# Performance work log

Hardware: AMD Instinct MI355X
Metric: run time of the kernel (lower is better)

The kernel has to match this reference:

```python
import jax, jax.numpy as jnp
import numpy as np

B, L, D = 8, 256, 32      # batch, key seq_len, input_dim
E, H, Q = 128, 8, 128     # embed_time, heads, num_query_steps
HID = 256                 # hidden_dim
V = 2 * D                 # value dim with mask channel
EK = E // H


def setup_inputs() -> dict:
    key = jax.random.key(0)
    ks = jax.random.split(key, 12)
    s = 0.05
    return {
        "values": jax.random.normal(ks[0], (B, L, D), jnp.float32),
        "mask": jax.random.randint(ks[1], (B, L, D), 0, 2).astype(jnp.int32),
        "times": jax.random.uniform(ks[2], (B, L), jnp.float32),
        # learn_time_embedding params (torch Linear(1, E-1) and Linear(1, 1))
        "w_per": jax.random.normal(ks[3], (1, E - 1), jnp.float32) * s,
        "b_per": jax.random.normal(ks[4], (E - 1,), jnp.float32) * s,
        "w_lin": jax.random.normal(ks[5], (1, 1), jnp.float32) * s,
        "b_lin": jax.random.normal(ks[6], (1,), jnp.float32) * s,
        # mTAND q/k linears (E,E) and output proj (HID, H*V)
        "wq": jax.random.normal(ks[7], (E, E), jnp.float32) * s,
        "bq": jnp.zeros((E,), jnp.float32),
        "wk": jax.random.normal(ks[8], (E, E), jnp.float32) * s,
        "bk": jnp.zeros((E,), jnp.float32),
        "wo": jax.random.normal(ks[9], (HID, H * V), jnp.float32) * s,
        "bo": jnp.zeros((HID,), jnp.float32),
        "ln_g": jnp.ones((HID,), jnp.float32),
        "ln_b": jnp.zeros((HID,), jnp.float32),
    }


def reference(values, mask, times, w_per, b_per, w_lin, b_lin,
              wq, bq, wk, bk, wo, bo, ln_g, ln_b):
    eps = 1e-6
    maskf = mask.astype(jnp.float32)                      # [B,L,D]
    obs = maskf.max(axis=-1) > 0                          # [B,L] observed steps
    # --- normalize times over observed steps ---
    tmin = jnp.where(obs, times, jnp.inf).min(axis=1, keepdims=True)
    tmax = jnp.where(obs, times, -jnp.inf).max(axis=1, keepdims=True)
    has = jnp.any(obs, axis=1, keepdims=True)             # [B,1]
    tmin = jnp.where(has, tmin, 0.0)
    tmax = jnp.where(has, tmax, 1.0)
    tn = (times - tmin) / jnp.maximum(tmax - tmin, eps)
    tn = jnp.where(obs, tn, 0.0)
    qt = jnp.broadcast_to(jnp.linspace(0.0, 1.0, Q, dtype=jnp.float32), (B, Q))

    def temb(tt):  # learnable time embedding: [linear(t), sin(periodic(t))]
        t = tt[..., None]                                 # [...,1]
        return jnp.concatenate([t @ w_lin.T + b_lin,
                                jnp.sin(t @ w_per + b_per)], axis=-1)

    tk = temb(tn)   # [B,L,E]
    tq = temb(qt)   # [B,Q,E]

    vinp = jnp.concatenate([values, maskf], axis=-1)      # [B,L,V]
    am = jnp.concatenate([maskf, maskf], axis=-1)         # [B,L,V]

    q = (tq @ wq.T + bq).reshape(B, Q, H, EK).transpose(0, 2, 1, 3)  # [B,H,Q,ek]
    k = (tk @ wk.T + bk).reshape(B, L, H, EK).transpose(0, 2, 1, 3)  # [B,H,L,ek]
    scores = jnp.einsum('bhqe,bhke->bhqk', q, k) / np.float32(np.sqrt(EK))
    # per-value-channel masked scores: [B,H,Q,L,V]
    s5 = jnp.where(am[:, None, None, :, :] == 0, jnp.float32(-10000.0),
                   scores[..., None])
    attn = jax.nn.softmax(s5, axis=-2)                    # softmax over L
    ctx = jnp.einsum('bhqkv,bkv->bhqv', attn, vinp)       # [B,H,Q,V]
    ctx = ctx.transpose(0, 2, 1, 3).reshape(B, Q, H * V)
    seq = ctx @ wo.T + bo                                 # [B,Q,HID]
    # LayerNorm (torch default eps=1e-5, biased var)
    mu = seq.mean(axis=-1, keepdims=True)
    var = ((seq - mu) ** 2).mean(axis=-1, keepdims=True)
    seq = (seq - mu) / jnp.sqrt(var + 1e-5) * ln_g + ln_b
    seq = seq * has.astype(jnp.float32)[:, :, None]       # zero seqs with no obs
    pooled = seq.mean(axis=1)
    return seq, pooled, qt
```

## Files before the change

### kernel.cpp

```cpp
#include <hip/hip_runtime.h>
#include <hip/hip_bf16.h>

#define B_   8
#define L_   256
#define D_   32
#define E_   128
#define H_   8
#define Q_   128
#define HID_ 256

__device__ __forceinline__ unsigned pack_bf2(float a, float b)
{
    __hip_bfloat16 ha = __float2bfloat16(a);
    __hip_bfloat16 hb = __float2bfloat16(b);
    unsigned short ua = *reinterpret_cast<unsigned short*>(&ha);
    unsigned short ub = *reinterpret_cast<unsigned short*>(&hb);
    return (unsigned)ua | ((unsigned)ub << 16);
}

__global__ __launch_bounds__(256) void k_prep1(
    const float* __restrict__ values, const int* __restrict__ mask,
    const float* __restrict__ times,
    float* __restrict__ tn, float* __restrict__ has,
    float* __restrict__ cm, float* __restrict__ colmean,
    float* __restrict__ mvm, unsigned* __restrict__ bitsT,
    float* __restrict__ qt_out, float* __restrict__ pooled)
{
    __shared__ float val_s[256][33];
    __shared__ unsigned bits_s[256];
    __shared__ float partial_s[8][32];
    __shared__ float sminw[4], smaxw[4];
    __shared__ float sh[2];

    int b = blockIdx.x;
    int t = threadIdx.x;

    const int*   mrow = mask   + (size_t)(b * L_ + t) * D_;
    const float* vrow = values + (size_t)(b * L_ + t) * D_;
    int4  m4[8];
    float4 v4[8];
    int any = 0;
    #pragma unroll
    for (int j = 0; j < 8; ++j) {
        m4[j] = reinterpret_cast<const int4*>(mrow)[j];
        v4[j] = reinterpret_cast<const float4*>(vrow)[j];
        any |= m4[j].x | m4[j].y | m4[j].z | m4[j].w;
        float4 mv;
        mv.x = m4[j].x ? v4[j].x : 0.f;
        mv.y = m4[j].y ? v4[j].y : 0.f;
        mv.z = m4[j].z ? v4[j].z : 0.f;
        mv.w = m4[j].w ? v4[j].w : 0.f;
        reinterpret_cast<float4*>(mvm + (size_t)(b * L_ + t) * D_)[j] = mv;
        val_s[t][j * 4 + 0] = v4[j].x;
        val_s[t][j * 4 + 1] = v4[j].y;
        val_s[t][j * 4 + 2] = v4[j].z;
        val_s[t][j * 4 + 3] = v4[j].w;
    }
    int wave = t >> 6;
    #pragma unroll
    for (int d = 0; d < D_; ++d) {
        int comp;
        { int j = d >> 2, c = d & 3;
          int4 mm = m4[j];
          comp = (c == 0) ? mm.x : (c == 1) ? mm.y : (c == 2) ? mm.z : mm.w; }
        unsigned long long bal = __ballot(comp != 0);
        if ((t & 63) == 0) {
            bits_s[d * 8 + wave * 2 + 0] = (unsigned)(bal & 0xffffffffull);
            bits_s[d * 8 + wave * 2 + 1] = (unsigned)(bal >> 32);
        }
    }
    float tv = times[b * L_ + t];
    {
        float wmin = any ? tv : 1e38f;
        float wmax = any ? tv : -1e38f;
        #pragma unroll
        for (int off = 32; off > 0; off >>= 1) {
            wmin = fminf(wmin, __shfl_xor(wmin, off));
            wmax = fmaxf(wmax, __shfl_xor(wmax, off));
        }
        if ((t & 63) == 0) { sminw[wave] = wmin; smaxw[wave] = wmax; }
    }
    {
        int d = t & 31, lg = t >> 5;
        float ps = 0.f;
        #pragma unroll
        for (int i = 0; i < 32; ++i) ps += val_s[lg * 32 + i][d];
        partial_s[lg][d] = ps;
    }
    __syncthreads();
    if (t == 0) {
        float mn = fminf(fminf(sminw[0], sminw[1]), fminf(sminw[2], sminw[3]));
        float mx = fmaxf(fmaxf(smaxw[0], smaxw[1]), fmaxf(smaxw[2], smaxw[3]));
        float hv = (mn < 1e37f) ? 1.f : 0.f;
        sh[0] = (hv > 0.f) ? mn : 0.f;
        sh[1] = (hv > 0.f) ? mx : 1.f;
        has[b] = hv;
    }
    __syncthreads();
    float inv = 1.f / fmaxf(sh[1] - sh[0], 1e-6f);
    tn[b * L_ + t] = any ? (tv - sh[0]) * inv : 0.f;

    if (t < Q_) qt_out[b * Q_ + t] = (float)t * (1.f / 127.f);
    pooled[b * HID_ + t] = 0.f;
    bitsT[b * 256 + t] = bits_s[t];

    if (t < D_) {
        float s = 0.f;
        #pragma unroll
        for (int lg = 0; lg < 8; ++lg) s += partial_s[lg][t];
        colmean[b * D_ + t] = s * (1.f / (float)L_);
        unsigned o = 0;
        #pragma unroll
        for (int w = 0; w < 8; ++w) o |= bits_s[t * 8 + w];
        cm[b * D_ + t] = o ? 1.f : 0.f;
    }
}

__global__ __launch_bounds__(256) void k_prep2(
    const float* __restrict__ tn, const float* __restrict__ cm,
    const float* __restrict__ w_per, const float* __restrict__ b_per,
    const float* __restrict__ w_lin, const float* __restrict__ b_lin,
    const float* __restrict__ wq, const float* __restrict__ bq,
    const float* __restrict__ wk, const float* __restrict__ bk,
    const float* __restrict__ wo, const float* __restrict__ bo,
    float* __restrict__ qproj, float* __restrict__ kproj,
    unsigned* __restrict__ wotvh, float* __restrict__ cvec)
{
    __shared__ __align__(16) float emb_q[2][E_];
    __shared__ __align__(16) float emb_k[8][E_];
    __shared__ float tsh[8];
    __shared__ float cm_s[D_];

    int blk = blockIdx.x;
    int t = threadIdx.x;

    if (blk < 64) {
        int half = t >> 7, e = t & 127;
        int q = blk * 2 + half;
        float tt = (float)q * (1.f / 127.f);
        emb_q[half][e] = (e == 0) ? (tt * w_lin[0] + b_lin[0])
                                  : __sinf(tt * w_per[e - 1] + b_per[e - 1]);
        __syncthreads();
        const float4* wr4 = reinterpret_cast<const float4*>(wq + (size_t)e * E_);
        const float4* e4  = reinterpret_cast<const float4*>(emb_q[half]);
        float acc = bq[e];
        #pragma unroll 8
        for (int j = 0; j < E_ / 4; ++j) {
            float4 w = wr4[j], x = e4[j];
            acc += w.x * x.x + w.y * x.y + w.z * x.z + w.w * x.w;
        }
        qproj[q * E_ + e] = acc;
    } else if (blk < 320) {
        int bl0 = (blk - 64) * 8;
        int e = t & 127, rh = t >> 7;
        if (t < 8) tsh[t] = tn[bl0 + t];
        __syncthreads();
        float wp = (e == 0) ? 0.f : w_per[e - 1];
        float bp = (e == 0) ? 0.f : b_per[e - 1];
        float wl = w_lin[0], bl = b_lin[0];
        #pragma unroll
        for (int rr = 0; rr < 4; ++rr) {
            int r = rh * 4 + rr;
            float tt = tsh[r];
            emb_k[r][e] = (e == 0) ? (tt * wl + bl) : __sinf(tt * wp + bp);
        }
        __syncthreads();
        const float4* wr4 = reinterpret_cast<const float4*>(wk + (size_t)e * E_);
        float bias = bk[e];
        float acc[4] = {bias, bias, bias, bias};
        #pragma unroll 8
        for (int j = 0; j < E_ / 4; ++j) {
            float4 w = wr4[j];
            #pragma unroll
            for (int rr = 0; rr < 4; ++rr) {
                float4 x = *reinterpret_cast<const float4*>(&emb_k[rh * 4 + rr][j * 4]);
                acc[rr] += w.x * x.x + w.y * x.y + w.z * x.z + w.w * x.w;
            }
        }
        #pragma unroll
        for (int rr = 0; rr < 4; ++rr)
            kproj[(size_t)(bl0 + rh * 4 + rr) * E_ + e] = acc[rr];
    } else if (blk < 352) {
        int c20 = (blk - 320) * 4;
        #pragma unroll
        for (int j = 0; j < 4; ++j) {
            int c2 = c20 + j;
            int ca = 2 * c2, cb = 2 * c2 + 1;
            int cola = (ca >> 5) * 64 + (ca & 31);
            int colb = (cb >> 5) * 64 + (cb & 31);
            float a = wo[(size_t)t * 512 + cola];
            float b = wo[(size_t)t * 512 + colb];
            wotvh[(size_t)c2 * HID_ + t] = pack_bf2(a, b);
        }
    } else {
        int b = blk - 352;
        if (t < D_) cm_s[t] = cm[b * D_ + t];
        __syncthreads();
        int hid = t;
        const float4* wrow4 = reinterpret_cast<const float4*>(wo + (size_t)hid * 512);
        float accm = 0.f;
        #pragma unroll
        for (int h1 = 0; h1 < 8; ++h1) {
            #pragma unroll
            for (int j = 0; j < 8; ++j) {
                float4 w = wrow4[h1 * 16 + 8 + j];
                accm += cm_s[j * 4 + 0] * w.x + cm_s[j * 4 + 1] * w.y
                      + cm_s[j * 4 + 2] * w.z + cm_s[j * 4 + 3] * w.w;
            }
        }
        cvec[b * HID_ + hid] = bo[hid] + accm;
    }
}

__global__ __launch_bounds__(256, 4) void k_main(
    const float* __restrict__ qproj, const float* __restrict__ kproj,
    const float* __restrict__ mvm, const unsigned* __restrict__ bitsT,
    const float* __restrict__ cm, const float* __restrict__ colmean,
    const unsigned* __restrict__ wotvh, const float* __restrict__ cvec,
    const float* __restrict__ has,
    const float* __restrict__ ln_g, const float* __restrict__ ln_b,
    float* __restrict__ seq_out, float* __restrict__ pooled)
{
    int q = blockIdx.x, b = blockIdx.y;
    int tid = threadIdx.x;
    __shared__ __align__(16) float e_s[L_ * H_];
    __shared__ __align__(16) float qv_s[E_];
    __shared__ unsigned bits_s[256];
    __shared__ float gmax_s[H_];
    __shared__ __align__(8) float ctx_s[256];
    __shared__ float red_s[8];
    __shared__ float mu_rs[2];

    bits_s[tid] = bitsT[b * 256 + tid];
    if (tid < E_) qv_s[tid] = qproj[q * E_ + tid];
    __syncthreads();

    const float4* kr4 = reinterpret_cast<const float4*>(kproj + (size_t)(b * L_ + tid) * E_);
    const float4* qv4 = reinterpret_cast<const float4*>(qv_s);
    float s[H_];
    #pragma unroll
    for (int h = 0; h < H_; ++h) {
        float acc = 0.f;
        #pragma unroll
        for (int j = 0; j < 4; ++j) {
            float4 kk = kr4[h * 4 + j], qq = qv4[h * 4 + j];
            acc += kk.x * qq.x + kk.y * qq.y + kk.z * qq.z + kk.w * qq.w;
        }
        s[h] = acc * 0.25f;
    }
    {
        float4* er4 = reinterpret_cast<float4*>(&e_s[tid * 8]);
        er4[0] = *reinterpret_cast<float4*>(&s[0]);
        er4[1] = *reinterpret_cast<float4*>(&s[4]);
    }
    __syncthreads();
    {
        int h = tid >> 5, ln = tid & 31;
        float mx = -1e30f;
        #pragma unroll
        for (int j = 0; j < 8; ++j) mx = fmaxf(mx, e_s[(ln + j * 32) * 8 + h]);
        #pragma unroll
        for (int off = 16; off > 0; off >>= 1) mx = fmaxf(mx, __shfl_xor(mx, off));
        if (ln == 0) gmax_s[h] = mx;
    }
    __syncthreads();
    {
        float e8[H_];
        #pragma unroll
        for (int h = 0; h < H_; ++h) e8[h] = __expf(s[h] - gmax_s[h]);
        float4* er4 = reinterpret_cast<float4*>(&e_s[tid * 8]);
        er4[0] = *reinterpret_cast<float4*>(&e8[0]);
        er4[1] = *reinterpret_cast<float4*>(&e8[4]);
    }
    __syncthreads();

    {
        int lseg = tid >> 6, h = (tid >> 3) & 7, d4 = tid & 7;
        unsigned w0[4], w1[4];
        #pragma unroll
        for (int j = 0; j < 4; ++j) {
            int d = d4 * 4 + j;
            w0[j] = bits_s[d * 8 + lseg * 2 + 0];
            w1[j] = bits_s[d * 8 + lseg * 2 + 1];
        }
        float4 av  = {0.f, 0.f, 0.f, 0.f};
        float4 den = {0.f, 0.f, 0.f, 0.f};
        const float4* mvg = reinterpret_cast<const float4*>(mvm + (size_t)b * L_ * D_);
        int l0 = lseg * 64;
        #pragma unroll 8
        for (int i = 0; i < 32; ++i) {
            int l = l0 + i;
            float e = e_s[l * 8 + h];
            float4 m = mvg[l * 8 + d4];
            av.x += e * m.x; av.y += e * m.y; av.z += e * m.z; av.w += e * m.w;
            den.x += ((w0[0] >> i) & 1u) ? e : 0.f;
            den.y += ((w0[1] >> i) & 1u) ? e : 0.f;
            den.z += ((w0[2] >> i) & 1u) ? e : 0.f;
            den.w += ((w0[3] >> i) & 1u) ? e : 0.f;
        }
        #pragma unroll 8
        for (int i = 0; i < 32; ++i) {
            int l = l0 + 32 + i;
            float e = e_s[l * 8 + h];
            float4 m = mvg[l * 8 + d4];
            av.x += e * m.x; av.y += e * m.y; av.z += e * m.z; av.w += e * m.w;
            den.x += ((w1[0] >> i) & 1u) ? e : 0.f;
            den.y += ((w1[1] >> i) & 1u) ? e : 0.f;
            den.z += ((w1[2] >> i) & 1u) ? e : 0.f;
            den.w += ((w1[3] >> i) & 1u) ? e : 0.f;
        }
        __syncthreads();
        float4* p4 = reinterpret_cast<float4*>(e_s);
        p4[tid * 2 + 0] = av;
        p4[tid * 2 + 1] = den;
    }
    __syncthreads();
    {
        int hh = tid >> 5, dd = tid & 31, dg = dd >> 2, jj = dd & 3;
        float a = 0.f, dn = 0.f;
        #pragma unroll
        for (int ls = 0; ls < 4; ++ls) {
            int pt = ls * 64 + hh * 8 + dg;
            a  += e_s[pt * 8 + jj];
            dn += e_s[pt * 8 + 4 + jj];
        }
        float cmf = cm[b * D_ + dd];
        ctx_s[tid] = (cmf > 0.f) ? (a / dn) : colmean[b * D_ + dd];
    }
    __syncthreads();

    int hid = tid;
    float acc = cvec[b * HID_ + hid];
    #pragma unroll 8
    for (int c2 = 0; c2 < 128; ++c2) {
        unsigned u = wotvh[(size_t)c2 * HID_ + hid];
        float2 cc = *reinterpret_cast<const float2*>(&ctx_s[c2 * 2]);
        float w0 = __uint_as_float(u << 16);
        float w1 = __uint_as_float(u & 0xffff0000u);
        acc += cc.x * w0 + cc.y * w1;
    }

    int wave = hid >> 6;
    {
        float sum = acc, ssum = acc * acc;
        #pragma unroll
        for (int off = 32; off > 0; off >>= 1) {
            sum  += __shfl_xor(sum, off);
            ssum += __shfl_xor(ssum, off);
        }
        if ((hid & 63) == 0) { red_s[wave] = sum; red_s[4 + wave] = ssum; }
    }
    __syncthreads();
    if (hid == 0) {
        float S  = red_s[0] + red_s[1] + red_s[2] + red_s[3];
        float SS = red_s[4] + red_s[5] + red_s[6] + red_s[7];
        float mu = S * (1.f / HID_);
        float var = SS * (1.f / HID_) - mu * mu;
        mu_rs[0] = mu;
        mu_rs[1] = rsqrtf(var + 1e-5f);
    }
    __syncthreads();

    float outv = ((acc - mu_rs[0]) * mu_rs[1] * ln_g[hid] + ln_b[hid]) * has[b];
    seq_out[((size_t)(b * Q_ + q)) * HID_ + hid] = outv;
    atomicAdd(&pooled[b * HID_ + hid], outv * (1.f / (float)Q_));
}

extern "C" void kernel_launch(void* const* d_in, const int* in_sizes, int n_in,
                              void* d_out, int out_size, void* d_ws, size_t ws_size,
                              hipStream_t stream)
{
    const float* values = (const float*)d_in[0];
    const int*   mask   = (const int*)  d_in[1];
    const float* times  = (const float*)d_in[2];
    const float* w_per  = (const float*)d_in[3];
    const float* b_per  = (const float*)d_in[4];
    const float* w_lin  = (const float*)d_in[5];
    const float* b_lin  = (const float*)d_in[6];
    const float* wq     = (const float*)d_in[7];
    const float* bq     = (const float*)d_in[8];
    const float* wk     = (const float*)d_in[9];
    const float* bk     = (const float*)d_in[10];
    const float* wo     = (const float*)d_in[11];
    const float* bo     = (const float*)d_in[12];
    const float* ln_g   = (const float*)d_in[13];
    const float* ln_b   = (const float*)d_in[14];

    float* out     = (float*)d_out;
    float* seq_out = out;
    float* pooled  = out + 262144;
    float* qt_out  = out + 262144 + 2048;

    float* ws         = (float*)d_ws;
    float*    tn      = ws;
    float*    has     = ws + 2048;
    float*    cm      = ws + 2056;
    float*    colmean = ws + 2312;
    float*    qproj   = ws + 2568;
    unsigned* bitsT   = (unsigned*)(ws + 18952);
    float*    mvm     = ws + 21000;
    float*    kproj   = ws + 86536;
    float*    cvec    = ws + 348680;
    unsigned* wotvh   = (unsigned*)(ws + 350728);

    k_prep1<<<B_,           256, 0, stream>>>(values, mask, times,
                 tn, has, cm, colmean, mvm, bitsT, qt_out, pooled);
    k_prep2<<<360,          256, 0, stream>>>(tn, cm, w_per, b_per, w_lin, b_lin,
                 wq, bq, wk, bk, wo, bo, qproj, kproj, wotvh, cvec);
    k_main <<<dim3(Q_, B_), 256, 0, stream>>>(qproj, kproj, mvm, bitsT,
                 cm, colmean, wotvh, cvec, has, ln_g, ln_b, seq_out, pooled);
}
```

Measured before the change: 144.1 us.

## Process two query steps per block and stage value matrix in shared memory

The main kernel now runs 512 threads per block, each half handling one query step, so the grid is halved. The per-batch masked value matrix (32 KB) is copied into LDS once per block and read from there in the context accumulation instead of from global memory. Shared buffers for scores, context and LayerNorm reductions are duplicated per query. This raises LDS use to about 50 KB per block, which may reduce occupancy, and every block still loads the full value tile, the same amount of work as before.

```diff
diff --git a/kernel.cpp b/kernel.cpp
--- a/kernel.cpp
+++ b/kernel.cpp
@@ -212,7 +212,7 @@
     }
 }
 
-__global__ __launch_bounds__(256, 4) void k_main(
+__global__ __launch_bounds__(512, 4) void k_main(
     const float* __restrict__ qproj, const float* __restrict__ kproj,
     const float* __restrict__ mvm, const unsigned* __restrict__ bitsT,
     const float* __restrict__ cm, const float* __restrict__ colmean,
@@ -221,22 +221,30 @@
     const float* __restrict__ ln_g, const float* __restrict__ ln_b,
     float* __restrict__ seq_out, float* __restrict__ pooled)
 {
-    int q = blockIdx.x, b = blockIdx.y;
+    int qb = blockIdx.x, b = blockIdx.y;
     int tid = threadIdx.x;
-    __shared__ __align__(16) float e_s[L_ * H_];
-    __shared__ __align__(16) float qv_s[E_];
+    int qi = tid >> 8, t = tid & 255;
+    __shared__ __align__(16) float mvm_s[L_ * D_];
+    __shared__ __align__(16) float e_s[2][L_ * H_];
+    __shared__ __align__(16) float qv_s[2][E_];
     __shared__ unsigned bits_s[256];
-    __shared__ float gmax_s[H_];
-    __shared__ __align__(8) float ctx_s[256];
-    __shared__ float red_s[8];
-    __shared__ float mu_rs[2];
-
-    bits_s[tid] = bitsT[b * 256 + tid];
-    if (tid < E_) qv_s[tid] = qproj[q * E_ + tid];
-    __syncthreads();
-
-    const float4* kr4 = reinterpret_cast<const float4*>(kproj + (size_t)(b * L_ + tid) * E_);
-    const float4* qv4 = reinterpret_cast<const float4*>(qv_s);
+    __shared__ float gmax_s[16];
+    __shared__ __align__(16) float ctx_s[2][256];
+    __shared__ float red_s[2][8];
+    __shared__ float mu_rs[2][2];
+
+    {
+        const float4* src = reinterpret_cast<const float4*>(mvm + (size_t)b * L_ * D_);
+        float4* dst = reinterpret_cast<float4*>(mvm_s);
+        #pragma unroll
+        for (int j = 0; j < 4; ++j) dst[tid + j * 512] = src[tid + j * 512];
+        if (qi == 0) bits_s[t] = bitsT[b * 256 + t];
+        if (t < E_) qv_s[qi][t] = qproj[(qb * 2 + qi) * E_ + t];
+    }
+    __syncthreads();
+
+    const float4* kr4 = reinterpret_cast<const float4*>(kproj + (size_t)(b * L_ + t) * E_);
+    const float4* qv4 = reinterpret_cast<const float4*>(qv_s[qi]);
     float s[H_];
     #pragma unroll
     for (int h = 0; h < H_; ++h) {
@@ -249,33 +257,34 @@
         s[h] = acc * 0.25f;
     }
     {
-        float4* er4 = reinterpret_cast<float4*>(&e_s[tid * 8]);
+        float4* er4 = reinterpret_cast<float4*>(&e_s[qi][t * 8]);
         er4[0] = *reinterpret_cast<float4*>(&s[0]);
         er4[1] = *reinterpret_cast<float4*>(&s[4]);
     }
     __syncthreads();
     {
-        int h = tid >> 5, ln = tid & 31;
+        int g = tid >> 5, ln = tid & 31;
+        int gq = g >> 3, h = g & 7;
         float mx = -1e30f;
         #pragma unroll
-        for (int j = 0; j < 8; ++j) mx = fmaxf(mx, e_s[(ln + j * 32) * 8 + h]);
+        for (int j = 0; j < 8; ++j) mx = fmaxf(mx, e_s[gq][(ln + j * 32) * 8 + h]);
         #pragma unroll
         for (int off = 16; off > 0; off >>= 1) mx = fmaxf(mx, __shfl_xor(mx, off));
-        if (ln == 0) gmax_s[h] = mx;
+        if (ln == 0) gmax_s[g] = mx;
     }
     __syncthreads();
     {
         float e8[H_];
         #pragma unroll
-        for (int h = 0; h < H_; ++h) e8[h] = __expf(s[h] - gmax_s[h]);
-        float4* er4 = reinterpret_cast<float4*>(&e_s[tid * 8]);
+        for (int h = 0; h < H_; ++h) e8[h] = __expf(s[h] - gmax_s[qi * 8 + h]);
+        float4* er4 = reinterpret_cast<float4*>(&e_s[qi][t * 8]);
         er4[0] = *reinterpret_cast<float4*>(&e8[0]);
         er4[1] = *reinterpret_cast<float4*>(&e8[4]);
     }
     __syncthreads();
 
     {
-        int lseg = tid >> 6, h = (tid >> 3) & 7, d4 = tid & 7;
+        int lseg = t >> 6, h = (t >> 3) & 7, d4 = t & 7;
         unsigned w0[4], w1[4];
         #pragma unroll
         for (int j = 0; j < 4; ++j) {
@@ -285,13 +294,14 @@
         }
         float4 av  = {0.f, 0.f, 0.f, 0.f};
         float4 den = {0.f, 0.f, 0.f, 0.f};
-        const float4* mvg = reinterpret_cast<const float4*>(mvm + (size_t)b * L_ * D_);
+        const float4* mv4 = reinterpret_cast<const float4*>(mvm_s);
+        const float* ep = e_s[qi];
         int l0 = lseg * 64;
         #pragma unroll 8
         for (int i = 0; i < 32; ++i) {
             int l = l0 + i;
-            float e = e_s[l * 8 + h];
-            float4 m = mvg[l * 8 + d4];
+            float e = ep[l * 8 + h];
+            float4 m = mv4[l * 8 + d4];
             av.x += e * m.x; av.y += e * m.y; av.z += e * m.z; av.w += e * m.w;
             den.x += ((w0[0] >> i) & 1u) ? e : 0.f;
             den.y += ((w0[1] >> i) & 1u) ? e : 0.f;
@@ -301,8 +311,8 @@
         #pragma unroll 8
         for (int i = 0; i < 32; ++i) {
             int l = l0 + 32 + i;
-            float e = e_s[l * 8 + h];
-            float4 m = mvg[l * 8 + d4];
+            float e = ep[l * 8 + h];
+            float4 m = mv4[l * 8 + d4];
             av.x += e * m.x; av.y += e * m.y; av.z += e * m.z; av.w += e * m.w;
             den.x += ((w1[0] >> i) & 1u) ? e : 0.f;
             den.y += ((w1[1] >> i) & 1u) ? e : 0.f;
@@ -310,37 +320,38 @@
             den.w += ((w1[3] >> i) & 1u) ? e : 0.f;
         }
         __syncthreads();
-        float4* p4 = reinterpret_cast<float4*>(e_s);
-        p4[tid * 2 + 0] = av;
-        p4[tid * 2 + 1] = den;
-    }
-    __syncthreads();
-    {
-        int hh = tid >> 5, dd = tid & 31, dg = dd >> 2, jj = dd & 3;
+        float4* p4 = reinterpret_cast<float4*>(e_s[qi]);
+        p4[t * 2 + 0] = av;
+        p4[t * 2 + 1] = den;
+    }
+    __syncthreads();
+    {
+        const float* part = e_s[qi];
+        int hh = t >> 5, dd = t & 31, dg = dd >> 2, jj = dd & 3;
         float a = 0.f, dn = 0.f;
         #pragma unroll
         for (int ls = 0; ls < 4; ++ls) {
             int pt = ls * 64 + hh * 8 + dg;
-            a  += e_s[pt * 8 + jj];
-            dn += e_s[pt * 8 + 4 + jj];
+            a  += part[pt * 8 + jj];
+            dn += part[pt * 8 + 4 + jj];
         }
         float cmf = cm[b * D_ + dd];
-        ctx_s[tid] = (cmf > 0.f) ? (a / dn) : colmean[b * D_ + dd];
-    }
-    __syncthreads();
-
-    int hid = tid;
+        ctx_s[qi][t] = (cmf > 0.f) ? (a / dn) : colmean[b * D_ + dd];
+    }
+    __syncthreads();
+
+    int hid = t;
     float acc = cvec[b * HID_ + hid];
     #pragma unroll 8
     for (int c2 = 0; c2 < 128; ++c2) {
         unsigned u = wotvh[(size_t)c2 * HID_ + hid];
-        float2 cc = *reinterpret_cast<const float2*>(&ctx_s[c2 * 2]);
+        float2 cc = *reinterpret_cast<const float2*>(&ctx_s[qi][c2 * 2]);
         float w0 = __uint_as_float(u << 16);
         float w1 = __uint_as_float(u & 0xffff0000u);
         acc += cc.x * w0 + cc.y * w1;
     }
 
-    int wave = hid >> 6;
+    int wave = tid >> 6;
     {
         float sum = acc, ssum = acc * acc;
         #pragma unroll
@@ -348,21 +359,24 @@
             sum  += __shfl_xor(sum, off);
             ssum += __shfl_xor(ssum, off);
         }
-        if ((hid & 63) == 0) { red_s[wave] = sum; red_s[4 + wave] = ssum; }
-    }
-    __syncthreads();
-    if (hid == 0) {
-        float S  = red_s[0] + red_s[1] + red_s[2] + red_s[3];
-        float SS = red_s[4] + red_s[5] + red_s[6] + red_s[7];
+        if ((tid & 63) == 0) {
+            red_s[qi][wave & 3]     = sum;
+            red_s[qi][4 + (wave & 3)] = ssum;
+        }
+    }
+    __syncthreads();
+    if (t == 0) {
+        float S  = red_s[qi][0] + red_s[qi][1] + red_s[qi][2] + red_s[qi][3];
+        float SS = red_s[qi][4] + red_s[qi][5] + red_s[qi][6] + red_s[qi][7];
         float mu = S * (1.f / HID_);
         float var = SS * (1.f / HID_) - mu * mu;
-        mu_rs[0] = mu;
-        mu_rs[1] = rsqrtf(var + 1e-5f);
-    }
-    __syncthreads();
-
-    float outv = ((acc - mu_rs[0]) * mu_rs[1] * ln_g[hid] + ln_b[hid]) * has[b];
-    seq_out[((size_t)(b * Q_ + q)) * HID_ + hid] = outv;
+        mu_rs[qi][0] = mu;
+        mu_rs[qi][1] = rsqrtf(var + 1e-5f);
+    }
+    __syncthreads();
+
+    float outv = ((acc - mu_rs[qi][0]) * mu_rs[qi][1] * ln_g[hid] + ln_b[hid]) * has[b];
+    seq_out[((size_t)(b * Q_ + qb * 2 + qi)) * HID_ + hid] = outv;
     atomicAdd(&pooled[b * HID_ + hid], outv * (1.f / (float)Q_));
 }
 
@@ -403,10 +417,10 @@
     float*    cvec    = ws + 348680;
     unsigned* wotvh   = (unsigned*)(ws + 350728);
 
-    k_prep1<<<B_,           256, 0, stream>>>(values, mask, times,
+    k_prep1<<<B_,               256, 0, stream>>>(values, mask, times,
                  tn, has, cm, colmean, mvm, bitsT, qt_out, pooled);
-    k_prep2<<<360,          256, 0, stream>>>(tn, cm, w_per, b_per, w_lin, b_lin,
+    k_prep2<<<360,              256, 0, stream>>>(tn, cm, w_per, b_per, w_lin, b_lin,
                  wq, bq, wk, bk, wo, bo, qproj, kproj, wotvh, cvec);
-    k_main <<<dim3(Q_, B_), 256, 0, stream>>>(qproj, kproj, mvm, bitsT,
+    k_main <<<dim3(Q_ / 2, B_), 512, 0, stream>>>(qproj, kproj, mvm, bitsT,
                  cm, colmean, wotvh, cvec, has, ln_g, ln_b, seq_out, pooled);
 }
```

Measured after the change: 137.8 us. 1.05x faster.
